# Kernel tuning notes

Measured on AMD Instinct MI355X. Metric: run time of the kernel, lower is better.

The kernel has to match this reference:

```python
import jax, jax.numpy as jnp
import numpy as np

B, L, T = 512, 1024, 128  # batch, seq_len, n_tags


def setup_inputs() -> dict:
    key = jax.random.key(0)
    k1, k2, k3 = jax.random.split(key, 3)
    return {
        "emit_scores": jax.random.normal(k1, (B, L, T), dtype=jnp.float32),
        "transitions": jax.random.normal(k2, (T, T), dtype=jnp.float32),
        "tag_weight": jax.random.uniform(k3, (T,), dtype=jnp.float32),
    }


def _viterbi_single(emit, transitions):
    # emit: [L, T] (already scaled by tag_weight); transitions: [T, T]
    def step(prev, obs):
        # scores[i, j] = prev[i] + obs[j] + transitions[i, j]
        scores = prev[:, None] + obs[None, :] + transitions  # [T, T]
        return jnp.max(scores, axis=0), jnp.argmax(scores, axis=0).astype(jnp.int32)

    prev, bps = jax.lax.scan(step, emit[0], emit[1:])  # bps: [L-1, T]
    best_score = jnp.max(prev)
    last = jnp.argmax(prev).astype(jnp.int32)

    # Backtrace: path[t] = bps[t][path[t+1]], path[L-1] = last
    def back(idx, bp):
        nidx = bp[idx]
        return nidx, nidx

    _, rev_path = jax.lax.scan(back, last, bps, reverse=True)  # [L-1]
    path = jnp.concatenate([rev_path, last[None]])  # [L]
    return path, best_score


def reference(emit_scores, transitions, tag_weight):
    # emit_scores *= tag_weight (broadcast over tag dim), matching the torch code
    emit = emit_scores * tag_weight  # [B, L, T]
    path, best_score = jax.vmap(_viterbi_single, in_axes=(0, None))(emit, transitions)
    # path: [B, L] int32 tag indices (the original maps these to tag strings);
    # best_score: [B] Viterbi max score.
    return path, best_score
```

## Files before the change

### kernel.cpp

```cpp
#include <hip/hip_runtime.h>

#define B 512
#define L 1024
#define T 128
#define NROWS (L - 1)
#define SEG 64
#define NSEG 16

typedef unsigned char u8;
typedef float f2 __attribute__((ext_vector_type(2)));

#define M3(a, b, c) fmaxf(fmaxf((a), (b)), (c))

static __device__ __forceinline__ f2 pkadd(f2 a, f2 b) {
    f2 d;
    asm("v_pk_add_f32 %0, %1, %2" : "=v"(d) : "v"(a), "v"(b));
    return d;
}
static __device__ __forceinline__ float mx3(float a, float b, float c) {
    float d;
    asm("v_max3_f32 %0, %1, %2, %3" : "=v"(d) : "v"(a), "v"(b), "v"(c));
    return d;
}

#define BAR()                                                  \
    do {                                                       \
        asm volatile("s_waitcnt lgkmcnt(0)" ::: "memory");     \
        __builtin_amdgcn_s_barrier();                          \
        asm volatile("" ::: "memory");                         \
    } while (0)


__global__ __launch_bounds__(512, 4) void viterbi_fwd_val(
    const float* __restrict__ emit, const float* __restrict__ trans,
    const float* __restrict__ w, float* __restrict__ out,
    float* __restrict__ prevws, int* __restrict__ lastTag)
{
    const int b   = blockIdx.x;
    const int tid = threadIdx.x;
    const int h   = tid & 3;
    const int j   = tid >> 2;
    const int hbase = h << 5;
    const bool lane0 = (h == 0);

    __shared__ __align__(16) float prevbuf[2 * T];
    __shared__ float swv[8];
    __shared__ int   swj[8];

    f2 tc2[16];
#pragma unroll
    for (int q = 0; q < 8; ++q) {
        f2 a, c;
        a.x = trans[(size_t)(hbase + 4 * q + 0) * T + j];
        a.y = trans[(size_t)(hbase + 4 * q + 1) * T + j];
        c.x = trans[(size_t)(hbase + 4 * q + 2) * T + j];
        c.y = trans[(size_t)(hbase + 4 * q + 3) * T + j];
        tc2[2 * q] = a; tc2[2 * q + 1] = c;
    }

    const float wj = w[j];
    const size_t ebase = (size_t)b * L * T;
    float* prow = prevws + (size_t)b * NROWS * T;

    const char* prd = (const char*)prevbuf + 128 * h;
    char* pwr = (char*)prevbuf + 16 * ((j >> 2) ^ (j >> 5)) + 4 * (j & 3);

    const float e0 = emit[ebase + j] * wj;
    if (lane0) *(float*)pwr = e0;
    if (h == 1) prow[j] = e0;
    float myprev = e0;
    float r_c = emit[ebase + (size_t)T + j];
    float r_1 = emit[ebase + (size_t)2 * T + j];
    float bv_prev = 0.0f;
    BAR();

#define SVX(K_) ((K_ & 1) ? sv[(K_) >> 1].y : sv[(K_) >> 1].x)
#define STEP(T_, ROFF_, WOFF_)                                                 \
    {                                                                          \
        const int t_ = (T_);                                                   \
        if (h == 1 && t_ >= 2)                                                 \
            prow[(size_t)(t_ - 1) * T + j] = bv_prev;                          \
        const int tn_ = (t_ + 2 < L) ? (t_ + 2) : (L - 1);                     \
        const float r_2 = emit[ebase + (size_t)tn_ * T + j];                   \
        const float obs_ = r_c * wj;                                           \
        f2 od_; od_.x = obs_; od_.y = obs_;                                    \
        f2 sv[16];                                                             \
        _Pragma("unroll")                                                      \
        for (int q = 0; q < 8; ++q) {                                          \
            const float4 p = *(const float4*)(prd + (ROFF_) + 16 * (q ^ h));   \
            f2 plo; plo.x = p.x; plo.y = p.y;                                  \
            f2 phi; phi.x = p.z; phi.y = p.w;                                  \
            sv[2 * q]     = pkadd(pkadd(plo, od_), tc2[2 * q]);                \
            sv[2 * q + 1] = pkadd(pkadd(phi, od_), tc2[2 * q + 1]);            \
        }                                                                      \
        const float m0 = mx3(SVX(0),  SVX(1),  SVX(2));                        \
        const float m1 = mx3(SVX(3),  SVX(4),  SVX(5));                        \
        const float m2 = mx3(SVX(6),  SVX(7),  SVX(8));                        \
        const float m3 = mx3(SVX(9),  SVX(10), SVX(11));                       \
        const float m4 = mx3(SVX(12), SVX(13), SVX(14));                       \
        const float m5 = mx3(SVX(15), SVX(16), SVX(17));                       \
        const float m6 = mx3(SVX(18), SVX(19), SVX(20));                       \
        const float m7 = mx3(SVX(21), SVX(22), SVX(23));                       \
        const float m8 = mx3(SVX(24), SVX(25), SVX(26));                       \
        const float m9 = mx3(SVX(27), SVX(28), SVX(29));                       \
        const float m10 = fmaxf(SVX(30), SVX(31));                             \
        const float n0 = mx3(m0, m1, m2);                                      \
        const float n1 = mx3(m3, m4, m5);                                      \
        const float n2 = mx3(m6, m7, m8);                                      \
        const float n3 = fmaxf(m9, m10);                                       \
        float bv = fmaxf(mx3(n0, n1, n2), n3);                                 \
        bv = fmaxf(bv, __shfl_xor(bv, 1));                                     \
        bv = fmaxf(bv, __shfl_xor(bv, 2));                                     \
        if (lane0) *(float*)(pwr + (WOFF_)) = bv;                              \
        myprev = bv;                                                           \
        bv_prev = bv;                                                          \
        r_c = r_1; r_1 = r_2;                                                  \
        BAR();                                                                 \
    }

    int t = 1;
    while (t + 1 < L) {
        STEP(t, 0, 512)
        STEP(t + 1, 512, 0)
        t += 2;
    }
    STEP(1023, 0, 512)
#undef STEP
#undef SVX

    float rv = myprev; int rj = j;
#pragma unroll
    for (int m = 4; m <= 32; m <<= 1) {
        const float pv = __shfl_xor(rv, m);
        const int   pj = __shfl_xor(rj, m);
        if (pv > rv || (pv == rv && pj < rj)) { rv = pv; rj = pj; }
    }
    if ((tid & 63) == 0) { swv[tid >> 6] = rv; swj[tid >> 6] = rj; }
    __syncthreads();
    if (tid == 0) {
        float fv = swv[0]; int fj = swj[0];
#pragma unroll
        for (int wv = 1; wv < 8; ++wv) {
            if (swv[wv] > fv || (swv[wv] == fv && swj[wv] < fj)) {
                fv = swv[wv]; fj = swj[wv];
            }
        }
        out[(size_t)B * L + b] = fv;
        out[(size_t)b * L + (L - 1)] = (float)fj;
        lastTag[b] = fj;
    }
}

__global__ __launch_bounds__(64, 1) void backtrace(
    const float* __restrict__ emit, const float* __restrict__ trans,
    const float* __restrict__ w, const float* __restrict__ prevws,
    const int* __restrict__ lastTag, float* __restrict__ out)
{
    const int b = blockIdx.x;
    const int lane = threadIdx.x;
    __shared__ float transT[T * T];

#pragma unroll 4
    for (int it = 0; it < (T * T) / 64; ++it) {
        const int k = it * 64 + lane;
        const int i = k >> 7, jj = k & 127;
        transT[jj * T + (i ^ (jj & 31))] = trans[k];
    }

    const float w0 = w[lane], w1 = w[lane + 64];
    const size_t pbase = (size_t)b * NROWS * T;
    const size_t ebase = (size_t)b * L * T;
    const size_t obase = (size_t)b * L;

    float rp0[8], rp1[8], re0[8], re1[8];
#pragma unroll
    for (int k = 0; k < 8; ++k) {
        rp0[k] = prevws[pbase + (size_t)(1022 - k) * T + lane];
        rp1[k] = prevws[pbase + (size_t)(1022 - k) * T + lane + 64];
        re0[k] = emit[ebase + (size_t)(1023 - k) * T + lane];
        re1[k] = emit[ebase + (size_t)(1023 - k) * T + lane + 64];
    }

    int idx = lastTag[b];
    const float bsc = out[(size_t)B * L + b];
    float pp0 = bsc, pp1 = bsc;
    __syncthreads();

    int r = 1022;

#define BODY(U_)                                                               \
    {                                                                          \
        const float c0_ = rp0[U_], c1_ = rp1[U_];                              \
        const float e0_ = re0[U_], e1_ = re1[U_];                              \
        const int pr = (r >= 8) ? (r - 8) : 0;                                 \
        rp0[U_] = prevws[pbase + (size_t)pr * T + lane];                       \
        rp1[U_] = prevws[pbase + (size_t)pr * T + lane + 64];                  \
        re0[U_] = emit[ebase + (size_t)(pr + 1) * T + lane];                   \
        re1[U_] = emit[ebase + (size_t)(pr + 1) * T + lane + 64];              \
        const int sl = idx & 63;                                               \
        const bool lo = idx < 64;                                              \
        const float bv  = __shfl(lo ? pp0 : pp1, sl);                          \
        const float ew0 = e0_ * w0, ew1 = e1_ * w1;                            \
        const float obs = __shfl(lo ? ew0 : ew1, sl);                          \
        const int xc = lane ^ (idx & 31);                                      \
        const float t0 = transT[idx * T + xc];                                 \
        const float t1 = transT[idx * T + 64 + xc];                            \
        const float s0 = (c0_ + obs) + t0;                                     \
        const float s1 = (c1_ + obs) + t1;                                     \
        const unsigned long long m0 = __ballot(s0 == bv);                      \
        const unsigned long long m1 = __ballot(s1 == bv);                      \
        idx = (m0 != 0ULL) ? __builtin_ctzll(m0)                               \
            : ((m1 != 0ULL) ? 64 + __builtin_ctzll(m1) : idx);                 \
        if (lane == 0) out[obase + r] = (float)idx;                            \
        pp0 = c0_; pp1 = c1_;                                                  \
        --r;                                                                   \
    }

#pragma unroll 1
    for (int g = 0; g < 127; ++g) {
        BODY(0) BODY(1) BODY(2) BODY(3) BODY(4) BODY(5) BODY(6) BODY(7)
    }
    BODY(0) BODY(1) BODY(2) BODY(3) BODY(4) BODY(5) BODY(6)
#undef BODY
}

__global__ __launch_bounds__(512, 4) void viterbi_fwd_slow(
    const float* __restrict__ emit, const float* __restrict__ trans,
    const float* __restrict__ w, float* __restrict__ out,
    u8* __restrict__ bps, int* __restrict__ lastTag)
{
    const int b   = blockIdx.x;
    const int tid = threadIdx.x;
    const int h   = tid & 3;
    const int j   = tid >> 2;
    const int hbase = h << 5;
    const bool lane0 = (h == 0);
    const int INF = 0x7fffffff;

    __shared__ __align__(16) float prevbuf[2 * T];
    __shared__ float swv[8];
    __shared__ int   swj[8];

    f2 tc2[16];
#pragma unroll
    for (int q = 0; q < 8; ++q) {
        f2 a, c;
        a.x = trans[(size_t)(hbase + 4 * q + 0) * T + j];
        a.y = trans[(size_t)(hbase + 4 * q + 1) * T + j];
        c.x = trans[(size_t)(hbase + 4 * q + 2) * T + j];
        c.y = trans[(size_t)(hbase + 4 * q + 3) * T + j];
        tc2[2 * q] = a; tc2[2 * q + 1] = c;
    }

    const float wj = w[j];
    const size_t ebase = (size_t)b * L * T;
    u8* bprow = bps + (size_t)b * NROWS * T;

    const char* prd = (const char*)prevbuf + 128 * h;
    char* pwr = (char*)prevbuf + 16 * ((j >> 2) ^ (j >> 5)) + 4 * (j & 3);

    const float e0 = emit[ebase + j] * wj;
    if (lane0) *(float*)pwr = e0;
    float myprev = e0;
    float raw_cur = emit[ebase + (size_t)T + j];
    int bidx_prev = 0;
    __syncthreads();

#define STEP(T_, ROFF_, WOFF_)                                                 \
    {                                                                          \
        const int t_ = (T_);                                                   \
        if (lane0 && t_ >= 2)                                                  \
            bprow[(size_t)(t_ - 2) * T + j] = (u8)bidx_prev;                   \
        const int tn_ = (t_ + 1 < L) ? (t_ + 1) : (L - 1);                     \
        const float raw_next_ = emit[ebase + (size_t)tn_ * T + j];             \
        const float obs_ = raw_cur * wj;                                       \
        f2 od_; od_.x = obs_; od_.y = obs_;                                    \
        f2 sv[16];                                                             \
        _Pragma("unroll")                                                      \
        for (int q = 0; q < 8; ++q) {                                          \
            const float4 p = *(const float4*)(prd + (ROFF_) + 16 * (q ^ h));   \
            f2 plo; plo.x = p.x; plo.y = p.y;                                  \
            f2 phi; phi.x = p.z; phi.y = p.w;                                  \
            sv[2 * q]     = (plo + od_) + tc2[2 * q];                          \
            sv[2 * q + 1] = (phi + od_) + tc2[2 * q + 1];                      \
        }                                                                      \
        float cm[4]; int loc[4];                                               \
        _Pragma("unroll")                                                      \
        for (int c = 0; c < 4; ++c) {                                          \
            const float s0 = sv[4 * c + 0].x, s1 = sv[4 * c + 0].y;            \
            const float s2 = sv[4 * c + 1].x, s3 = sv[4 * c + 1].y;            \
            const float s4 = sv[4 * c + 2].x, s5 = sv[4 * c + 2].y;            \
            const float s6 = sv[4 * c + 3].x, s7 = sv[4 * c + 3].y;            \
            const float m = M3(M3(s0, s1, s2), M3(s3, s4, s5),                 \
                               fmaxf(s6, s7));                                 \
            int k = 0;                                                         \
            k = (s7 == m) ? 7 : k; k = (s6 == m) ? 6 : k;                      \
            k = (s5 == m) ? 5 : k; k = (s4 == m) ? 4 : k;                      \
            k = (s3 == m) ? 3 : k; k = (s2 == m) ? 2 : k;                      \
            k = (s1 == m) ? 1 : k;                                             \
            cm[c] = m; loc[c] = 8 * c + k;                                     \
        }                                                                      \
        float bv = fmaxf(fmaxf(cm[0], cm[1]), fmaxf(cm[2], cm[3]));            \
        const int l0 = (cm[0] == bv) ? loc[0] : INF;                           \
        const int l1 = (cm[1] == bv) ? loc[1] : INF;                           \
        const int l2 = (cm[2] == bv) ? loc[2] : INF;                           \
        const int l3 = (cm[3] == bv) ? loc[3] : INF;                           \
        const int lm = min(min(min(l0, l1), l2), l3);                          \
        int gi = hbase + lm;                                                   \
        const float lv = bv;                                                   \
        bv = fmaxf(bv, __shfl_xor(bv, 1));                                     \
        bv = fmaxf(bv, __shfl_xor(bv, 2));                                     \
        int ii = (lv == bv) ? gi : INF;                                        \
        ii = min(ii, __shfl_xor(ii, 1));                                       \
        ii = min(ii, __shfl_xor(ii, 2));                                       \
        if (lane0) *(float*)(pwr + (WOFF_)) = bv;                              \
        myprev = bv;                                                           \
        bidx_prev = ii;                                                        \
        raw_cur = raw_next_;                                                   \
        __syncthreads();                                                       \
    }

    int t = 1;
    while (t + 1 < L) {
        STEP(t, 0, 512)
        STEP(t + 1, 512, 0)
        t += 2;
    }
    STEP(1023, 0, 512)
#undef STEP

    if (lane0) bprow[(size_t)(NROWS - 1) * T + j] = (u8)bidx_prev;

    float rv = myprev; int rj = j;
#pragma unroll
    for (int m = 4; m <= 32; m <<= 1) {
        const float pv = __shfl_xor(rv, m);
        const int   pj = __shfl_xor(rj, m);
        if (pv > rv || (pv == rv && pj < rj)) { rv = pv; rj = pj; }
    }
    if ((tid & 63) == 0) { swv[tid >> 6] = rv; swj[tid >> 6] = rj; }
    __syncthreads();
    if (tid == 0) {
        float fv = swv[0]; int fj = swj[0];
#pragma unroll
        for (int wv = 1; wv < 8; ++wv) {
            if (swv[wv] > fv || (swv[wv] == fv && swj[wv] < fj)) {
                fv = swv[wv]; fj = swj[wv];
            }
        }
        out[(size_t)B * L + b] = fv;
        out[(size_t)b * L + (L - 1)] = (float)fj;
        lastTag[b] = fj;
    }
}

__global__ __launch_bounds__(T) void segcomp(const u8* __restrict__ bps,
                                             u8* __restrict__ comp)
{
    const int s = blockIdx.x & (NSEG - 1);
    const int b = blockIdx.x >> 4;
    const int r0 = s * SEG;
    const int cnt = (NROWS - r0 < SEG) ? (NROWS - r0) : SEG;

    __shared__ __align__(16) u8 rows[SEG * T];
    const uint4* src = (const uint4*)(bps + ((size_t)b * NROWS + r0) * T);
    uint4* dst = (uint4*)rows;
    const int nvec = cnt * (T / 16);
    for (int k = threadIdx.x; k < nvec; k += T) dst[k] = src[k];
    __syncthreads();

    int x = threadIdx.x;
    for (int k = cnt - 1; k >= 0; --k) x = rows[k * T + x];
    comp[((size_t)b * NSEG + s) * T + threadIdx.x] = (u8)x;
}

__global__ void chainseg(const u8* __restrict__ comp,
                         const int* __restrict__ lastTag,
                         float* __restrict__ out)
{
    const int b = blockIdx.x * blockDim.x + threadIdx.x;
    if (b >= B) return;
    int e = lastTag[b];
#pragma unroll 1
    for (int s = NSEG - 1; s >= 0; --s) {
        e = comp[((size_t)b * NSEG + s) * T + e];
        out[(size_t)b * L + s * SEG] = (float)e;
    }
}

__global__ __launch_bounds__(T) void fillseg(const u8* __restrict__ bps,
                                             const int* __restrict__ lastTag,
                                             float* __restrict__ out)
{
    const int s = blockIdx.x & (NSEG - 1);
    const int b = blockIdx.x >> 4;
    const int r0 = s * SEG;
    const int cnt = (NROWS - r0 < SEG) ? (NROWS - r0) : SEG;

    __shared__ __align__(16) u8 rows[SEG * T];
    const uint4* src = (const uint4*)(bps + ((size_t)b * NROWS + r0) * T);
    uint4* dst = (uint4*)rows;
    const int nvec = cnt * (T / 16);
    for (int k = threadIdx.x; k < nvec; k += T) dst[k] = src[k];
    __syncthreads();

    if (threadIdx.x == 0) {
        int e = (s == NSEG - 1) ? lastTag[b]
                                : (int)out[(size_t)b * L + (size_t)(s + 1) * SEG];
        for (int k = cnt - 1; k >= 1; --k) {
            e = rows[k * T + e];
            out[(size_t)b * L + r0 + k] = (float)e;
        }
    }
}

extern "C" void kernel_launch(void* const* d_in, const int* in_sizes, int n_in,
                              void* d_out, int out_size, void* d_ws, size_t ws_size,
                              hipStream_t stream)
{
    const float* emit  = (const float*)d_in[0];
    const float* trans = (const float*)d_in[1];
    const float* w     = (const float*)d_in[2];
    float* out = (float*)d_out;

    const size_t prev_bytes = (size_t)B * NROWS * T * sizeof(float);
    const size_t need_fast  = prev_bytes + B * sizeof(int);

    if (ws_size >= need_fast) {
        float* prevws  = (float*)d_ws;
        int*   lastTag = (int*)((char*)d_ws + prev_bytes);
        viterbi_fwd_val<<<B, 512, 0, stream>>>(emit, trans, w, out, prevws, lastTag);
        backtrace<<<B, 64, 0, stream>>>(emit, trans, w, prevws, lastTag, out);
    } else {
        u8*  bps     = (u8*)d_ws;
        u8*  comp    = bps + (size_t)B * NROWS * T;
        int* lastTag = (int*)(comp + (size_t)B * NSEG * T);
        viterbi_fwd_slow<<<B, 512, 0, stream>>>(emit, trans, w, out, bps, lastTag);
        segcomp<<<B * NSEG, T, 0, stream>>>(bps, comp);
        chainseg<<<2, 256, 0, stream>>>(comp, lastTag, out);
        fillseg<<<B * NSEG, T, 0, stream>>>(bps, lastTag, out);
    }
}
```

Baseline: 867.4 us.

## Halve forward block size, each thread computes two tag columns reusing prev loads

The forward Viterbi kernel now runs 256 threads per batch row instead of 512, with each thread group handling two destination tags (j and j+64). The shared-memory prev vector slice is loaded once and reused for both columns, halving LDS reads per output and the number of waves hitting each barrier. In exchange each thread holds twice the transition registers (64 floats) and does twice the ALU work per step, which lengthens the serial per-step critical path and may lower occupancy.

Measured after the change: 864.2 us. Within noise of the previous version (-0.4%).

```diff
diff --git a/kernel.cpp b/kernel.cpp
--- a/kernel.cpp
+++ b/kernel.cpp
@@ -31,7 +31,7 @@
     } while (0)
 
 
-__global__ __launch_bounds__(512, 4) void viterbi_fwd_val(
+__global__ __launch_bounds__(256, 2) void viterbi_fwd_val(
     const float* __restrict__ emit, const float* __restrict__ trans,
     const float* __restrict__ w, float* __restrict__ out,
     float* __restrict__ prevws, int* __restrict__ lastTag)
@@ -44,10 +44,10 @@
     const bool lane0 = (h == 0);
 
     __shared__ __align__(16) float prevbuf[2 * T];
-    __shared__ float swv[8];
-    __shared__ int   swj[8];
-
-    f2 tc2[16];
+    __shared__ float swv[4];
+    __shared__ int   swj[4];
+
+    f2 tca[16], tcb[16];
 #pragma unroll
     for (int q = 0; q < 8; ++q) {
         f2 a, c;
@@ -55,44 +55,62 @@
         a.y = trans[(size_t)(hbase + 4 * q + 1) * T + j];
         c.x = trans[(size_t)(hbase + 4 * q + 2) * T + j];
         c.y = trans[(size_t)(hbase + 4 * q + 3) * T + j];
-        tc2[2 * q] = a; tc2[2 * q + 1] = c;
-    }
-
-    const float wj = w[j];
+        tca[2 * q] = a; tca[2 * q + 1] = c;
+    }
+#pragma unroll
+    for (int q = 0; q < 8; ++q) {
+        f2 a, c;
+        a.x = trans[(size_t)(hbase + 4 * q + 0) * T + j + 64];
+        a.y = trans[(size_t)(hbase + 4 * q + 1) * T + j + 64];
+        c.x = trans[(size_t)(hbase + 4 * q + 2) * T + j + 64];
+        c.y = trans[(size_t)(hbase + 4 * q + 3) * T + j + 64];
+        tcb[2 * q] = a; tcb[2 * q + 1] = c;
+    }
+
+    const float w0 = w[j], w1 = w[j + 64];
     const size_t ebase = (size_t)b * L * T;
     float* prow = prevws + (size_t)b * NROWS * T;
 
     const char* prd = (const char*)prevbuf + 128 * h;
-    char* pwr = (char*)prevbuf + 16 * ((j >> 2) ^ (j >> 5)) + 4 * (j & 3);
-
-    const float e0 = emit[ebase + j] * wj;
-    if (lane0) *(float*)pwr = e0;
-    if (h == 1) prow[j] = e0;
-    float myprev = e0;
-    float r_c = emit[ebase + (size_t)T + j];
-    float r_1 = emit[ebase + (size_t)2 * T + j];
-    float bv_prev = 0.0f;
+    const int wo0 = 16 * ((j >> 2) ^ (j >> 5)) + 4 * (j & 3);
+    const int jj = j + 64;
+    const int wo1 = 16 * ((jj >> 2) ^ (jj >> 5)) + 4 * (jj & 3);
+    char* pw0 = (char*)prevbuf + wo0;
+    char* pw1 = (char*)prevbuf + wo1;
+
+    const float e0a = emit[ebase + j] * w0;
+    const float e0b = emit[ebase + jj] * w1;
+    if (lane0) { *(float*)pw0 = e0a; *(float*)pw1 = e0b; }
+    if (h == 1) { prow[j] = e0a; prow[jj] = e0b; }
+    float mA = e0a, mB = e0b;
+    float rc0 = emit[ebase + (size_t)T + j];
+    float rc1 = emit[ebase + (size_t)T + jj];
+    float r10 = emit[ebase + (size_t)2 * T + j];
+    float r11 = emit[ebase + (size_t)2 * T + jj];
+    float bpA = 0.0f, bpB = 0.0f;
     BAR();
 
 #define SVX(K_) ((K_ & 1) ? sv[(K_) >> 1].y : sv[(K_) >> 1].x)
-#define STEP(T_, ROFF_, WOFF_)                                                 \
+#define COLMAX(TC_, OD_, BV_)                                                  \
+    float BV_;                                                                 \
     {                                                                          \
-        const int t_ = (T_);                                                   \
-        if (h == 1 && t_ >= 2)                                                 \
-            prow[(size_t)(t_ - 1) * T + j] = bv_prev;                          \
-        const int tn_ = (t_ + 2 < L) ? (t_ + 2) : (L - 1);                     \
-        const float r_2 = emit[ebase + (size_t)tn_ * T + j];                   \
-        const float obs_ = r_c * wj;                                           \
-        f2 od_; od_.x = obs_; od_.y = obs_;                                    \
         f2 sv[16];                                                             \
-        _Pragma("unroll")                                                      \
-        for (int q = 0; q < 8; ++q) {                                          \
-            const float4 p = *(const float4*)(prd + (ROFF_) + 16 * (q ^ h));   \
-            f2 plo; plo.x = p.x; plo.y = p.y;                                  \
-            f2 phi; phi.x = p.z; phi.y = p.w;                                  \
-            sv[2 * q]     = pkadd(pkadd(plo, od_), tc2[2 * q]);                \
-            sv[2 * q + 1] = pkadd(pkadd(phi, od_), tc2[2 * q + 1]);            \
-        }                                                                      \
+        sv[0]  = pkadd(pkadd(g0, OD_), TC_[0]);                                \
+        sv[1]  = pkadd(pkadd(g1, OD_), TC_[1]);                                \
+        sv[2]  = pkadd(pkadd(g2, OD_), TC_[2]);                                \
+        sv[3]  = pkadd(pkadd(g3, OD_), TC_[3]);                                \
+        sv[4]  = pkadd(pkadd(g4, OD_), TC_[4]);                                \
+        sv[5]  = pkadd(pkadd(g5, OD_), TC_[5]);                                \
+        sv[6]  = pkadd(pkadd(g6, OD_), TC_[6]);                                \
+        sv[7]  = pkadd(pkadd(g7, OD_), TC_[7]);                                \
+        sv[8]  = pkadd(pkadd(g8, OD_), TC_[8]);                                \
+        sv[9]  = pkadd(pkadd(g9, OD_), TC_[9]);                                \
+        sv[10] = pkadd(pkadd(g10, OD_), TC_[10]);                              \
+        sv[11] = pkadd(pkadd(g11, OD_), TC_[11]);                              \
+        sv[12] = pkadd(pkadd(g12, OD_), TC_[12]);                              \
+        sv[13] = pkadd(pkadd(g13, OD_), TC_[13]);                              \
+        sv[14] = pkadd(pkadd(g14, OD_), TC_[14]);                              \
+        sv[15] = pkadd(pkadd(g15, OD_), TC_[15]);                              \
         const float m0 = mx3(SVX(0),  SVX(1),  SVX(2));                        \
         const float m1 = mx3(SVX(3),  SVX(4),  SVX(5));                        \
         const float m2 = mx3(SVX(6),  SVX(7),  SVX(8));                        \
@@ -108,13 +126,61 @@
         const float n1 = mx3(m3, m4, m5);                                      \
         const float n2 = mx3(m6, m7, m8);                                      \
         const float n3 = fmaxf(m9, m10);                                       \
-        float bv = fmaxf(mx3(n0, n1, n2), n3);                                 \
-        bv = fmaxf(bv, __shfl_xor(bv, 1));                                     \
-        bv = fmaxf(bv, __shfl_xor(bv, 2));                                     \
-        if (lane0) *(float*)(pwr + (WOFF_)) = bv;                              \
-        myprev = bv;                                                           \
-        bv_prev = bv;                                                          \
-        r_c = r_1; r_1 = r_2;                                                  \
+        BV_ = fmaxf(mx3(n0, n1, n2), n3);                                      \
+    }
+
+#define STEP(T_, ROFF_, WOFF_)                                                 \
+    {                                                                          \
+        const int t_ = (T_);                                                   \
+        if (h == 1 && t_ >= 2) {                                               \
+            prow[(size_t)(t_ - 1) * T + j]  = bpA;                             \
+            prow[(size_t)(t_ - 1) * T + jj] = bpB;                             \
+        }                                                                      \
+        const int tn_ = (t_ + 2 < L) ? (t_ + 2) : (L - 1);                     \
+        const float r20 = emit[ebase + (size_t)tn_ * T + j];                   \
+        const float r21 = emit[ebase + (size_t)tn_ * T + jj];                  \
+        const float4 p0 = *(const float4*)(prd + (ROFF_) + 16 * (0 ^ h));      \
+        const float4 p1 = *(const float4*)(prd + (ROFF_) + 16 * (1 ^ h));      \
+        const float4 p2 = *(const float4*)(prd + (ROFF_) + 16 * (2 ^ h));      \
+        const float4 p3 = *(const float4*)(prd + (ROFF_) + 16 * (3 ^ h));      \
+        const float4 p4 = *(const float4*)(prd + (ROFF_) + 16 * (4 ^ h));      \
+        const float4 p5 = *(const float4*)(prd + (ROFF_) + 16 * (5 ^ h));      \
+        const float4 p6 = *(const float4*)(prd + (ROFF_) + 16 * (6 ^ h));      \
+        const float4 p7 = *(const float4*)(prd + (ROFF_) + 16 * (7 ^ h));      \
+        f2 g0;  g0.x  = p0.x; g0.y  = p0.y;                                    \
+        f2 g1;  g1.x  = p0.z; g1.y  = p0.w;                                    \
+        f2 g2;  g2.x  = p1.x; g2.y  = p1.y;                                    \
+        f2 g3;  g3.x  = p1.z; g3.y  = p1.w;                                    \
+        f2 g4;  g4.x  = p2.x; g4.y  = p2.y;                                    \
+        f2 g5;  g5.x  = p2.z; g5.y  = p2.w;                                    \
+        f2 g6;  g6.x  = p3.x; g6.y  = p3.y;                                    \
+        f2 g7;  g7.x  = p3.z; g7.y  = p3.w;                                    \
+        f2 g8;  g8.x  = p4.x; g8.y  = p4.y;                                    \
+        f2 g9;  g9.x  = p4.z; g9.y  = p4.w;                                    \
+        f2 g10; g10.x = p5.x; g10.y = p5.y;                                    \
+        f2 g11; g11.x = p5.z; g11.y = p5.w;                                    \
+        f2 g12; g12.x = p6.x; g12.y = p6.y;                                    \
+        f2 g13; g13.x = p6.z; g13.y = p6.w;                                    \
+        f2 g14; g14.x = p7.x; g14.y = p7.y;                                    \
+        f2 g15; g15.x = p7.z; g15.y = p7.w;                                    \
+        const float obs0 = rc0 * w0, obs1 = rc1 * w1;                          \
+        f2 od0; od0.x = obs0; od0.y = obs0;                                    \
+        f2 od1; od1.x = obs1; od1.y = obs1;                                    \
+        COLMAX(tca, od0, bvA0)                                                 \
+        COLMAX(tcb, od1, bvB0)                                                 \
+        float bvA = bvA0, bvB = bvB0;                                          \
+        bvA = fmaxf(bvA, __shfl_xor(bvA, 1));                                  \
+        bvB = fmaxf(bvB, __shfl_xor(bvB, 1));                                  \
+        bvA = fmaxf(bvA, __shfl_xor(bvA, 2));                                  \
+        bvB = fmaxf(bvB, __shfl_xor(bvB, 2));                                  \
+        if (lane0) {                                                           \
+            *(float*)(pw0 + (WOFF_)) = bvA;                                    \
+            *(float*)(pw1 + (WOFF_)) = bvB;                                    \
+        }                                                                      \
+        mA = bvA; mB = bvB;                                                    \
+        bpA = bvA; bpB = bvB;                                                  \
+        rc0 = r10; r10 = r20;                                                  \
+        rc1 = r11; r11 = r21;                                                  \
         BAR();                                                                 \
     }
 
@@ -126,9 +192,11 @@
     }
     STEP(1023, 0, 512)
 #undef STEP
+#undef COLMAX
 #undef SVX
 
-    float rv = myprev; int rj = j;
+    float rv; int rj;
+    if (mB > mA) { rv = mB; rj = jj; } else { rv = mA; rj = j; }
 #pragma unroll
     for (int m = 4; m <= 32; m <<= 1) {
         const float pv = __shfl_xor(rv, m);
@@ -140,7 +208,7 @@
     if (tid == 0) {
         float fv = swv[0]; int fj = swj[0];
 #pragma unroll
-        for (int wv = 1; wv < 8; ++wv) {
+        for (int wv = 1; wv < 4; ++wv) {
             if (swv[wv] > fv || (swv[wv] == fv && swj[wv] < fj)) {
                 fv = swv[wv]; fj = swj[wv];
             }
@@ -429,7 +497,7 @@
     if (ws_size >= need_fast) {
         float* prevws  = (float*)d_ws;
         int*   lastTag = (int*)((char*)d_ws + prev_bytes);
-        viterbi_fwd_val<<<B, 512, 0, stream>>>(emit, trans, w, out, prevws, lastTag);
+        viterbi_fwd_val<<<B, 256, 0, stream>>>(emit, trans, w, out, prevws, lastTag);
         backtrace<<<B, 64, 0, stream>>>(emit, trans, w, prevws, lastTag, out);
     } else {
         u8*  bps     = (u8*)d_ws;
```
